# Performance work log

Hardware: AMD Instinct MI355X
Metric: run time of the kernel (lower is better)

The kernel has to match this reference:

```python
import jax, jax.numpy as jnp
import numpy as np

B, L = 8, 2048
H_IN = 20
K1, K2 = 16, 32
NG = 32            # n_gaussians
D1, D2 = 7, 5      # gaussian kernel input dims
DM = 128           # outer product out_features
DH = 32            # attribute embedding out_features
IDX_MAX = 8.0      # index_distance_max


def _gather(x, idx):
    # x: (B,L,H), idx: (B,L,K) -> (B,L,K,H)
    b = jnp.arange(x.shape[0])[:, None, None]
    return x[b, idx]


def _neighbors(frames, kmax):
    c = frames[:, :, 0, :]                      # centers (B,L,3)
    sq = jnp.sum(c * c, axis=-1)
    d2 = sq[:, :, None] + sq[:, None, :] - 2.0 * jnp.einsum('bld,bmd->blm', c, c)
    _, idx = jax.lax.top_k(-d2, kmax)           # self (d2=0) lands in slot 0
    return idx


def _coords(frames, seq_idx, idx):
    c = frames[:, :, 0, :]
    axes = frames[:, :, 1:4, :]                 # local frame axes of center node
    z = frames[:, :, 3, :]
    c_j = _gather(c, idx)
    z_j = _gather(z, idx)
    delta = c_j - c[:, :, None, :]              # (B,L,K,3)
    dist = jnp.sqrt(jnp.sum(delta * delta, -1, keepdims=True) + 1e-12)
    eucl = jnp.einsum('blkd,blad->blka', delta, axes)   # neighbor coords in local frame
    zdotz = jnp.sum(z[:, :, None, :] * z_j, -1, keepdims=True)
    deltadotz = jnp.sum(delta * z_j, -1, keepdims=True) / dist
    zdotdelta = jnp.sum(z[:, :, None, :] * delta, -1, keepdims=True) / dist
    sidx = seq_idx.astype(jnp.float32)          # (B,L,1)
    idist = jnp.clip(jnp.abs(_gather(sidx, idx) - sidx[:, :, None, :]), 0.0, IDX_MAX)
    return eucl, dist, zdotz, deltadotz, zdotdelta, idist


def _gaussian(x, centers, prec):
    # full-covariance Gaussian kernel: exp(-0.5 ||P_n (x - mu_n)||^2)
    diff = x[..., None] - centers               # (...,d,NG)
    y = jnp.einsum('...dn,dkn->...kn', diff, prec)
    return jnp.exp(-0.5 * jnp.sum(y * y, axis=-2))


def _forward(aa_attributes, aa_frame, aa_indices,
             gk1_centers, gk1_prec, op_kernel, op_bias,
             emb_W, emb_b, beta_W, beta_b, selfatt_W, selfatt_b,
             crossatt_W, crossatt_b, nodef_W, nodef_b,
             gk2_centers, gk2_prec, emb2_W, emb2_b):
    # --- neighborhood 1: euclidian + index_distance + ZdotZ + (DeltadotZ,ZdotDelta)
    idx1 = _neighbors(aa_frame, K1)
    eucl, _, zz, dz, zd, idist = _coords(aa_frame, aa_indices, idx1)
    coords1 = jnp.concatenate([eucl, idist, zz, dz, zd], axis=-1)   # (B,L,K1,7)
    neigh_attr = _gather(aa_attributes, idx1)                        # (B,L,K1,20)
    g1 = _gaussian(coords1, gk1_centers, gk1_prec)                   # (B,L,K1,NG)
    # outer-product embedding: sum over neighbors and (gaussian x attribute) pairs
    filt = jnp.einsum('blkg,blkh,gho->blo', g1, neigh_attr, op_kernel) + op_bias
    f = jax.nn.relu(filt)                                            # (B,L,128)
    emb = jax.nn.relu(f @ emb_W + emb_b)                             # (B,L,32)
    beta = jax.nn.relu(emb @ beta_W + beta_b)                        # (B,L,1)
    satt = jax.nn.relu(emb @ selfatt_W + selfatt_b)                  # (B,L,1)
    catt = jax.nn.relu(emb @ crossatt_W + crossatt_b)                # (B,L,1)
    nodef = jax.nn.relu(emb @ nodef_W + nodef_b)                     # (B,L,2)
    # --- neighborhood 2: distance + ZdotZ + (DeltadotZ,ZdotDelta) + index_distance
    idx2 = _neighbors(aa_frame, K2)
    _, dist2, zz2, dz2, zd2, idist2 = _coords(aa_frame, aa_indices, idx2)
    coords2 = jnp.concatenate([dist2, zz2, dz2, zd2, idist2], axis=-1)  # (B,L,K2,5)
    att_local = _gather(catt, idx2)                                  # (B,L,K2,1)
    nodef_local = _gather(nodef, idx2)                               # (B,L,K2,2)
    g2 = _gaussian(coords2, gk2_centers, gk2_prec)                   # (B,L,K2,NG)
    gw = jax.nn.relu(g2 @ emb2_W + emb2_b)                           # (B,L,K2,1)
    # --- graph attention aggregation (self slot is k=0)
    e = att_local.at[:, :, 0, :].set(satt)
    logits = beta[:, :, None, :] * e
    logits = logits - jnp.max(logits, axis=2, keepdims=True)
    w = gw * jnp.exp(logits)
    a = w / (jnp.sum(w, axis=2, keepdims=True) + 1e-6)               # (B,L,K2,1)
    out = jnp.sum(a * nodef_local, axis=2)                           # (B,L,2)
    return out


def setup_inputs():
    key = jax.random.key(0)
    ks = jax.random.split(key, 16)
    eye1 = jnp.tile(jnp.eye(D1, dtype=jnp.float32)[:, :, None], (1, 1, NG))
    eye2 = jnp.tile(jnp.eye(D2, dtype=jnp.float32)[:, :, None], (1, 1, NG))
    return {
        'aa_attributes': jax.random.normal(ks[0], (B, L, H_IN), jnp.float32),
        'aa_frame': jax.random.normal(ks[1], (B, L, 4, 3), jnp.float32),
        'aa_indices': jnp.arange(B * L, dtype=jnp.int32).reshape(B, L, 1),
        'gk1_centers': 0.1 * jax.random.normal(ks[2], (D1, NG), jnp.float32),
        'gk1_prec': eye1 + 0.05 * jax.random.normal(ks[3], (D1, D1, NG), jnp.float32),
        'op_kernel': 0.05 * jax.random.normal(ks[4], (NG, H_IN, DM), jnp.float32),
        'op_bias': jnp.zeros((DM,), jnp.float32),
        'emb_W': jax.random.normal(ks[5], (DM, DH), jnp.float32) / np.sqrt(DM),
        'emb_b': jnp.zeros((DH,), jnp.float32),
        'beta_W': jax.random.normal(ks[6], (DH, 1), jnp.float32) / np.sqrt(DH),
        'beta_b': jnp.zeros((1,), jnp.float32),
        'selfatt_W': jax.random.normal(ks[7], (DH, 1), jnp.float32) / np.sqrt(DH),
        'selfatt_b': jnp.zeros((1,), jnp.float32),
        'crossatt_W': jax.random.normal(ks[8], (DH, 1), jnp.float32) / np.sqrt(DH),
        'crossatt_b': jnp.zeros((1,), jnp.float32),
        'nodef_W': jax.random.normal(ks[9], (DH, 2), jnp.float32) / np.sqrt(DH),
        'nodef_b': jnp.zeros((2,), jnp.float32),
        'gk2_centers': 0.1 * jax.random.normal(ks[10], (D2, NG), jnp.float32),
        'gk2_prec': eye2 + 0.05 * jax.random.normal(ks[11], (D2, D2, NG), jnp.float32),
        'emb2_W': jax.random.normal(ks[12], (NG, 1), jnp.float32) / np.sqrt(NG),
        'emb2_b': jnp.zeros((1,), jnp.float32),
    }


def reference(aa_attributes, aa_frame, aa_indices,
              gk1_centers, gk1_prec, op_kernel, op_bias,
              emb_W, emb_b, beta_W, beta_b, selfatt_W, selfatt_b,
              crossatt_W, crossatt_b, nodef_W, nodef_b,
              gk2_centers, gk2_prec, emb2_W, emb2_b):
    return _forward(aa_attributes, aa_frame, aa_indices,
                    gk1_centers, gk1_prec, op_kernel, op_bias,
                    emb_W, emb_b, beta_W, beta_b, selfatt_W, selfatt_b,
                    crossatt_W, crossatt_b, nodef_W, nodef_b,
                    gk2_centers, gk2_prec, emb2_W, emb2_b)
```

## Files before the change

### kernel.cpp

```cpp
#include <hip/hip_runtime.h>

typedef unsigned int u32;
typedef unsigned long long u64;
typedef unsigned short u16;

#define NL 2048

typedef __attribute__((ext_vector_type(8))) short bf16x8;
typedef __attribute__((ext_vector_type(16))) float f32x16;

__device__ __forceinline__ u16 to_bf16(float f) {
  u32 b = __float_as_uint(f);
  b += 0x7FFFu + ((b >> 16) & 1u);
  return (u16)(b >> 16);
}

__device__ __forceinline__ void gload_lds16(const void* g, void* l) {
  __builtin_amdgcn_global_load_lds(
      (const __attribute__((address_space(1))) u32*)g,
      (__attribute__((address_space(3))) u32*)l, 16, 0, 0);
}

__device__ __forceinline__ u32 sort64_u32(u32 v, int lane) {
#pragma unroll
  for (int k = 2; k <= 64; k <<= 1) {
#pragma unroll
    for (int j = k >> 1; j > 0; j >>= 1) {
      u32 p = (u32)__shfl_xor((int)v, j, 64);
      bool lower = ((lane & j) == 0);
      bool asc = ((lane & k) == 0);
      u32 lo = v < p ? v : p;
      u32 hi = v < p ? p : v;
      v = (lower == asc) ? lo : hi;
    }
  }
  return v;
}

__global__ __launch_bounds__(512) void knn_prep_kernel(
    const float* __restrict__ frames, int* __restrict__ idx32,
    const float* __restrict__ opW, const float* __restrict__ embW,
    const float* __restrict__ betaW, const float* __restrict__ sattW,
    const float* __restrict__ cattW, const float* __restrict__ nodW,
    const float* __restrict__ betaB, const float* __restrict__ sattB,
    const float* __restrict__ cattB, const float* __restrict__ nodB,
    u16* __restrict__ opWt, u16* __restrict__ embWt, float* __restrict__ w5,
    float* __restrict__ b5) {
  __shared__ union U {
    struct {
      float4 cand[2048];
      u64 comp[8][256];
    } k;
    float tp[128 * 73];
  } sm;
  const int bx = blockIdx.x;
  const int tid = threadIdx.x;

  if (bx >= 2048) {
    if (bx < 2058) {
      const int k0 = (bx - 2048) * 64;
#pragma unroll
      for (int j = 0; j < 4; j++) {
        int f = tid + j * 512;
        int kk = f >> 5;
        int o4 = (f & 31) * 4;
        float4 v = *(const float4*)(opW + (size_t)(k0 + kk) * 128 + o4);
        sm.tp[(o4 + 0) * 73 + kk] = v.x;
        sm.tp[(o4 + 1) * 73 + kk] = v.y;
        sm.tp[(o4 + 2) * 73 + kk] = v.z;
        sm.tp[(o4 + 3) * 73 + kk] = v.w;
      }
      __syncthreads();
      u32* ow = (u32*)opWt;
#pragma unroll
      for (int j = 0; j < 8; j++) {
        int f = tid + j * 512;
        int o = f >> 5, q = f & 31;
        float lo = sm.tp[o * 73 + q * 2];
        float hi = sm.tp[o * 73 + q * 2 + 1];
        ow[o * 320 + (k0 >> 1) + q] = (u32)to_bf16(lo) | ((u32)to_bf16(hi) << 16);
      }
    } else {
      for (int f = tid; f < 4096; f += 512) {
        int j = f >> 7, kk = f & 127;
        embWt[f] = to_bf16(embW[(size_t)kk * 32 + j]);
      }
      if (tid < 160) {
        int h = tid >> 5, j = tid & 31;
        float v = (h == 0) ? betaW[j]
                  : (h == 1) ? sattW[j]
                  : (h == 2) ? cattW[j]
                  : (h == 3) ? nodW[j * 2]
                             : nodW[j * 2 + 1];
        w5[j * 8 + h] = v;
      } else if (tid < 165) {
        int h = tid - 160;
        float v = (h == 0) ? betaB[0]
                  : (h == 1) ? sattB[0]
                  : (h == 2) ? cattB[0]
                  : (h == 3) ? nodB[0]
                             : nodB[1];
        b5[h] = v;
      }
    }
    return;
  }

  const int w = tid >> 6, lane = tid & 63;
  const int query = bx * 8 + w;
  const int b = query >> 11, lq = query & (NL - 1);

#pragma unroll
  for (int i = 0; i < 4; i++) {
    int l = tid + i * 512;
    const float* fp = frames + (size_t)(b * NL + l) * 12;
    float4 fr = *(const float4*)fp;
    sm.k.cand[l] = make_float4(fr.x, fr.y, fr.z,
                               fr.x * fr.x + fr.y * fr.y + fr.z * fr.z);
  }
  __syncthreads();

  float4 me = sm.k.cand[lq];
  u32 k[32];
  u32 m = 0xFFFFFFFFu;
#pragma unroll
  for (int i = 0; i < 32; i++) {
    float4 c = sm.k.cand[i * 64 + lane];
    float dot = c.x * me.x + c.y * me.y + c.z * me.z;
    float d2 = (me.w + c.w) - 2.0f * dot;
    u32 kb = __float_as_uint(d2);
    u32 key = kb ^ ((u32)((int)kb >> 31) | 0x80000000u);
    k[i] = key;
    m = key < m ? key : m;
  }

  u32 ms = sort64_u32(m, lane);
  u32 T0 = (u32)__shfl((int)ms, 31, 64);

  int base = 0;
#pragma unroll
  for (int i = 0; i < 32; i++) {
    bool flag = (k[i] <= T0);
    u64 mask = __ballot(flag);
    if (flag) {
      u32 rank = __builtin_amdgcn_mbcnt_hi(
          (u32)(mask >> 32), __builtin_amdgcn_mbcnt_lo((u32)mask, 0u));
      int pos = base + (int)rank;
      if (pos < 256) sm.k.comp[w][pos] = ((u64)k[i] << 32) | (u32)(i * 64 + lane);
    }
    base += (int)__popcll(mask);
  }
  int cnt = base < 256 ? base : 256;
  __syncthreads();

  for (int b0 = 0; b0 < cnt; b0 += 64) {
    bool live = (b0 + lane < cnt);
    u64 e = live ? sm.k.comp[w][b0 + lane] : ~0ull;
    int r = 0;
    for (int mi = 0; mi < cnt; mi++) {
      u64 em = sm.k.comp[w][mi];
      r += (em < e) ? 1 : 0;
    }
    if (live && r < 32)
      idx32[(size_t)query * 32 + r] = (int)(e & 0xFFFFFFFFull);
  }
}

__global__ __launch_bounds__(256) void stage1_kernel(
    const float* __restrict__ frames, const float* __restrict__ attrs,
    const int* __restrict__ aaidx, const float* __restrict__ cen1,
    const float* __restrict__ prec1, const int* __restrict__ idx32,
    u16* __restrict__ outer) {
  __shared__ float sCoord[4 * 16 * 8];
  __shared__ float sAttrT[4 * 20 * 16];
  __shared__ float sG1T[4 * 32 * 17];
  const int tid = threadIdx.x;
  const int pt = tid >> 6, lane = tid & 63;
  const int pid = blockIdx.x * 4 + pt;
  const int b = pid >> 11;
  const int g = lane & 31;

  float pr[7][7], cn[7];
#pragma unroll
  for (int d = 0; d < 7; d++) {
    cn[d] = cen1[d * 32 + g];
#pragma unroll
    for (int kk = 0; kk < 7; kk++) pr[d][kk] = prec1[(d * 7 + kk) * 32 + g];
  }

  if (lane < 16) {
    int n = lane;
    int j = idx32[pid * 32 + n];
    int jg = b * NL + j;
    const float* fs = frames + (size_t)pid * 12;
    const float* fj = frames + (size_t)jg * 12;
    float4 A0 = *(const float4*)(fs);
    float4 A1 = *(const float4*)(fs + 4);
    float4 A2 = *(const float4*)(fs + 8);
    float4 B0 = *(const float4*)(fj);
    float4 B2 = *(const float4*)(fj + 8);
    float dx = B0.x - A0.x, dy = B0.y - A0.y, dzc = B0.z - A0.z;
    float a0x = A0.w, a0y = A1.x, a0z = A1.y;
    float a1x = A1.z, a1y = A1.w, a1z = A2.x;
    float a2x = A2.y, a2y = A2.z, a2z = A2.w;
    float zjx = B2.y, zjy = B2.z, zjz = B2.w;
    float dd = dx * dx + dy * dy + dzc * dzc + 1e-12f;
    float dist = sqrtf(dd);
    float e0 = dx * a0x + dy * a0y + dzc * a0z;
    float e1 = dx * a1x + dy * a1y + dzc * a1z;
    float e2 = dx * a2x + dy * a2y + dzc * a2z;
    float zz = a2x * zjx + a2y * zjy + a2z * zjz;
    float dzv = (dx * zjx + dy * zjy + dzc * zjz) / dist;
    float zdv = (a2x * dx + a2y * dy + a2z * dzc) / dist;
    float si = (float)aaidx[pid];
    float sj = (float)aaidx[jg];
    float idist = fminf(fabsf(sj - si), 8.0f);
    float* cr = sCoord + pt * 128 + n * 8;
    cr[0] = e0; cr[1] = e1; cr[2] = e2; cr[3] = idist;
    cr[4] = zz; cr[5] = dzv; cr[6] = zdv;
    const float* ar = attrs + (size_t)jg * 20;
    float4 q0 = *(const float4*)(ar);
    float4 q1 = *(const float4*)(ar + 4);
    float4 q2 = *(const float4*)(ar + 8);
    float4 q3 = *(const float4*)(ar + 12);
    float4 q4 = *(const float4*)(ar + 16);
    float av[20] = {q0.x, q0.y, q0.z, q0.w, q1.x, q1.y, q1.z, q1.w,
                    q2.x, q2.y, q2.z, q2.w, q3.x, q3.y, q3.z, q3.w,
                    q4.x, q4.y, q4.z, q4.w};
#pragma unroll
    for (int h = 0; h < 20; h++) sAttrT[pt * 320 + h * 16 + n] = av[h];
  }
  __syncthreads();
  {
    const int nh = lane >> 5;
#pragma unroll
    for (int i = 0; i < 8; i++) {
      int n = nh * 8 + i;
      const float* cr = sCoord + pt * 128 + n * 8;
      float df[7];
#pragma unroll
      for (int d = 0; d < 7; d++) df[d] = cr[d] - cn[d];
      float s = 0.0f;
#pragma unroll
      for (int kk = 0; kk < 7; kk++) {
        float y = 0.0f;
#pragma unroll
        for (int d = 0; d < 7; d++) y = fmaf(df[d], pr[d][kk], y);
        s = fmaf(y, y, s);
      }
      sG1T[pt * 544 + g * 17 + n] = __expf(-0.5f * s);
    }
  }
  __syncthreads();
  {
    const int hg = lane >> 5;
    float g16[16];
#pragma unroll
    for (int n = 0; n < 16; n++) g16[n] = sG1T[pt * 544 + g * 17 + n];
    u32* orow = (u32*)(outer + (size_t)pid * 640) + (g * 20 + hg * 10) / 2;
#pragma unroll
    for (int i = 0; i < 5; i++) {
      int h0 = hg * 10 + i * 2, h1 = h0 + 1;
      float a0 = 0.f, a1 = 0.f;
#pragma unroll
      for (int c = 0; c < 4; c++) {
        float4 v0 = *(float4*)&sAttrT[pt * 320 + h0 * 16 + c * 4];
        float4 v1 = *(float4*)&sAttrT[pt * 320 + h1 * 16 + c * 4];
        a0 = fmaf(v0.x, g16[c * 4 + 0], a0);
        a0 = fmaf(v0.y, g16[c * 4 + 1], a0);
        a0 = fmaf(v0.z, g16[c * 4 + 2], a0);
        a0 = fmaf(v0.w, g16[c * 4 + 3], a0);
        a1 = fmaf(v1.x, g16[c * 4 + 0], a1);
        a1 = fmaf(v1.y, g16[c * 4 + 1], a1);
        a1 = fmaf(v1.z, g16[c * 4 + 2], a1);
        a1 = fmaf(v1.w, g16[c * 4 + 3], a1);
      }
      orow[i] = (u32)to_bf16(a0) | ((u32)to_bf16(a1) << 16);
    }
  }
}

__global__ __launch_bounds__(256) void gemm_kernel(
    const u16* __restrict__ outer,
    const u16* __restrict__ opWt,
    const float* __restrict__ opB,
    const u16* __restrict__ embWt,
    const float* __restrict__ embB,
    const float* __restrict__ w5,
    const float* __restrict__ b5,
    float* __restrict__ head8) {
  __shared__ char smem[40960];
  const int tid = threadIdx.x;
  const int w = tid >> 6, lane = tid & 63;
  const int p0 = blockIdx.x * 32;
  const int lr = lane >> 3, lc = lane & 7;
  const int gsw = lc ^ lr;
  const int m = lane & 31, kh = lane >> 5;

  f32x16 acc;
#pragma unroll
  for (int r = 0; r < 16; r++) acc[r] = 0.f;

  const u16* gA = outer + (size_t)(p0 + w * 8 + lr) * 640 + gsw * 8;
#pragma unroll
  for (int cc = 0; cc < 10; cc++)
    gload_lds16(gA + cc * 64, smem + cc * 4096 + w * 1024);
  __syncthreads();

  const u16* gB = opWt + (size_t)(w * 32 + m) * 640;
#pragma unroll
  for (int cc = 0; cc < 10; cc++) {
#pragma unroll
    for (int s = 0; s < 4; s++) {
      int pg = (s * 2 + kh) ^ (m & 7);
      bf16x8 av = *(bf16x8*)(smem + cc * 4096 + m * 128 + pg * 16);
      bf16x8 bv = *(const bf16x8*)(gB + cc * 64 + s * 16 + kh * 8);
      acc = __builtin_amdgcn_mfma_f32_32x32x16_bf16(av, bv, acc, 0, 0, 0);
    }
  }
  __syncthreads();

  const int o = w * 32 + m;
  float bo = opB[o];
#pragma unroll
  for (int i = 0; i < 2; i++) {
    int j = w * 8 + i * 4 + (lane >> 4);
    int ge = (lane & 15) ^ (j & 7);
    gload_lds16(embWt + j * 128 + ge * 8, smem + 8192 + w * 2048 + i * 1024);
  }
  u16* sFb = (u16*)smem;
#pragma unroll
  for (int r = 0; r < 16; r++) {
    int mm = (r & 3) + 8 * (r >> 2) + 4 * kh;
    float v = fmaxf(acc[r] + bo, 0.f);
    int pg = (o >> 3) ^ (mm & 7);
    sFb[mm * 128 + pg * 8 + (o & 7)] = to_bf16(v);
  }
  __syncthreads();

  f32x16 acc2;
#pragma unroll
  for (int r = 0; r < 16; r++) acc2[r] = 0.f;
#pragma unroll
  for (int t2 = 0; t2 < 2; t2++) {
    int gg = (w * 2 + t2) * 2 + kh;
    int pg = gg ^ (m & 7);
    bf16x8 av = *(bf16x8*)(smem + m * 256 + pg * 16);
    bf16x8 bv = *(bf16x8*)(smem + 8192 + m * 256 + pg * 16);
    acc2 = __builtin_amdgcn_mfma_f32_32x32x16_bf16(av, bv, acc2, 0, 0, 0);
  }
  float* scr = (float*)(smem + 16384) + w * 1024;
#pragma unroll
  for (int r = 0; r < 16; r++) {
    int mm = (r & 3) + 8 * (r >> 2) + 4 * kh;
    scr[mm * 32 + m] = acc2[r];
  }
  __syncthreads();

  {
    float* sc = (float*)(smem + 16384);
    int i4 = tid * 4;
    float4 v0 = *(float4*)(sc + i4);
    float4 v1 = *(float4*)(sc + 1024 + i4);
    float4 v2 = *(float4*)(sc + 2048 + i4);
    float4 v3 = *(float4*)(sc + 3072 + i4);
    int pp = tid >> 3, j0 = (tid & 7) * 4;
    float4 eb = *(const float4*)(embB + j0);
    float4 e;
    e.x = fmaxf(v0.x + v1.x + v2.x + v3.x + eb.x, 0.f);
    e.y = fmaxf(v0.y + v1.y + v2.y + v3.y + eb.y, 0.f);
    e.z = fmaxf(v0.z + v1.z + v2.z + v3.z + eb.z, 0.f);
    e.w = fmaxf(v0.w + v1.w + v2.w + v3.w + eb.w, 0.f);
    *(float4*)((float*)smem + pp * 36 + j0) = e;
  }
  __syncthreads();

  if (tid < 160) {
    int h = tid >> 5, p = tid & 31;
    const float* sE = (const float*)smem + p * 36;
    float a = b5[h];
#pragma unroll
    for (int j = 0; j < 32; j++) a = fmaf(sE[j], w5[j * 8 + h], a);
    a = fmaxf(a, 0.f);
    int slot = (h < 2) ? (h + 4) : (h - 2);
    head8[(size_t)(p0 + p) * 8 + slot] = a;
  }
}

__global__ __launch_bounds__(256) void stage2_kernel(
    const float* __restrict__ frames, const int* __restrict__ aaidx,
    const float* __restrict__ cen2, const float* __restrict__ prec2,
    const float* __restrict__ emb2W, const float* __restrict__ emb2B,
    const int* __restrict__ idx32, const float* __restrict__ head8,
    float* __restrict__ out) {
  __shared__ float sCoord[4 * 32 * 5];
  __shared__ float sG2[4 * 32 * 33];
  const int tid = threadIdx.x;
  const int pt = tid >> 6, lane = tid & 63;
  const int pid = blockIdx.x * 4 + pt;
  const int b = pid >> 11;
  const int g = lane & 31;

  float pr[5][5], cn[5];
#pragma unroll
  for (int d = 0; d < 5; d++) {
    cn[d] = cen2[d * 32 + g];
#pragma unroll
    for (int kk = 0; kk < 5; kk++) pr[d][kk] = prec2[(d * 5 + kk) * 32 + g];
  }

  float4 hv = make_float4(0.f, 0.f, 0.f, 0.f);
  float betaS = 0.f, sattS = 0.f;
  if (lane < 32) {
    int n = lane;
    int j = idx32[pid * 32 + n];
    int jg = b * NL + j;
    const float* fs = frames + (size_t)pid * 12;
    const float* fj = frames + (size_t)jg * 12;
    float4 A0 = *(const float4*)(fs);
    float4 A2 = *(const float4*)(fs + 8);
    float4 B0 = *(const float4*)(fj);
    float4 B2 = *(const float4*)(fj + 8);
    float dx = B0.x - A0.x, dy = B0.y - A0.y, dzc = B0.z - A0.z;
    float a2x = A2.y, a2y = A2.z, a2z = A2.w;
    float zjx = B2.y, zjy = B2.z, zjz = B2.w;
    float dd = dx * dx + dy * dy + dzc * dzc + 1e-12f;
    float dist = sqrtf(dd);
    float zz = a2x * zjx + a2y * zjy + a2z * zjz;
    float dzv = (dx * zjx + dy * zjy + dzc * zjz) / dist;
    float zdv = (a2x * dx + a2y * dy + a2z * dzc) / dist;
    float si = (float)aaidx[pid];
    float sj = (float)aaidx[jg];
    float idist = fminf(fabsf(sj - si), 8.0f);
    float* cr = sCoord + pt * 160 + n * 5;
    cr[0] = dist; cr[1] = zz; cr[2] = dzv; cr[3] = zdv; cr[4] = idist;
    hv = *(const float4*)(head8 + (size_t)jg * 8);
    betaS = head8[(size_t)pid * 8 + 4];
    sattS = head8[(size_t)pid * 8 + 5];
  }
  __syncthreads();
  {
    const int nh = lane >> 5;
#pragma unroll
    for (int i = 0; i < 16; i++) {
      int n = nh * 16 + i;
      const float* cr = sCoord + pt * 160 + n * 5;
      float df[5];
#pragma unroll
      for (int d = 0; d < 5; d++) df[d] = cr[d] - cn[d];
      float s = 0.0f;
#pragma unroll
      for (int kk = 0; kk < 5; kk++) {
        float y = 0.0f;
#pragma unroll
        for (int d = 0; d < 5; d++) y = fmaf(df[d], pr[d][kk], y);
        s = fmaf(y, y, s);
      }
      sG2[pt * 1056 + n * 33 + g] = __expf(-0.5f * s);
    }
  }
  __syncthreads();
  if (lane < 32) {
    int n = lane;
    float gw = emb2B[0];
#pragma unroll 8
    for (int gg = 0; gg < 32; gg++)
      gw = fmaf(sG2[pt * 1056 + n * 33 + gg], emb2W[gg], gw);
    gw = fmaxf(gw, 0.0f);
    float e = (n == 0) ? sattS : hv.x;
    float logit = betaS * e;
    float mx = logit;
#pragma unroll
    for (int d = 1; d < 32; d <<= 1) mx = fmaxf(mx, __shfl_xor(mx, d, 64));
    float wv = gw * __expf(logit - mx);
    float S = wv;
#pragma unroll
    for (int d = 1; d < 32; d <<= 1) S += __shfl_xor(S, d, 64);
    float a = wv / (S + 1e-6f);
    float o0 = a * hv.y, o1 = a * hv.z;
#pragma unroll
    for (int d = 1; d < 32; d <<= 1) {
      o0 += __shfl_xor(o0, d, 64);
      o1 += __shfl_xor(o1, d, 64);
    }
    if (n == 0) {
      out[pid * 2 + 0] = o0;
      out[pid * 2 + 1] = o1;
    }
  }
}

extern "C" void kernel_launch(void* const* d_in, const int* in_sizes, int n_in,
                              void* d_out, int out_size, void* d_ws, size_t ws_size,
                              hipStream_t stream) {
  const float* attrs = (const float*)d_in[0];
  const float* frames = (const float*)d_in[1];
  const int* aaidx = (const int*)d_in[2];
  const float* cen1 = (const float*)d_in[3];
  const float* prec1 = (const float*)d_in[4];
  const float* opW = (const float*)d_in[5];
  const float* opB = (const float*)d_in[6];
  const float* embW = (const float*)d_in[7];
  const float* embB = (const float*)d_in[8];
  const float* betaW = (const float*)d_in[9];
  const float* betaB = (const float*)d_in[10];
  const float* sattW = (const float*)d_in[11];
  const float* sattB = (const float*)d_in[12];
  const float* cattW = (const float*)d_in[13];
  const float* cattB = (const float*)d_in[14];
  const float* nodW = (const float*)d_in[15];
  const float* nodB = (const float*)d_in[16];
  const float* cen2 = (const float*)d_in[17];
  const float* prec2 = (const float*)d_in[18];
  const float* emb2W = (const float*)d_in[19];
  const float* emb2B = (const float*)d_in[20];
  float* out = (float*)d_out;

  char* ws = (char*)d_ws;
  int* idx32 = (int*)ws;
  u16* outer_bf = (u16*)(ws + 2097152);
  float* head8 = (float*)(ws + 23068672);
  u16* opWt = (u16*)(ws + 23592960);
  u16* embWt = (u16*)(ws + 23756800);
  float* w5 = (float*)(ws + 23764992);
  float* b5 = (float*)(ws + 23766016);

  knn_prep_kernel<<<dim3(2059), dim3(512), 0, stream>>>(
      frames, idx32, opW, embW, betaW, sattW, cattW, nodW, betaB, sattB,
      cattB, nodB, opWt, embWt, w5, b5);
  stage1_kernel<<<dim3(4096), dim3(256), 0, stream>>>(frames, attrs, aaidx, cen1,
                                                      prec1, idx32, outer_bf);
  gemm_kernel<<<dim3(512), dim3(256), 0, stream>>>(outer_bf, opWt, opB, embWt,
                                                   embB, w5, b5, head8);
  stage2_kernel<<<dim3(4096), dim3(256), 0, stream>>>(frames, aaidx, cen2, prec2,
                                                      emb2W, emb2B, idx32, head8, out);
}
```

Measured before the change: 184.1 us.

## Fuse stage1 outer-product build into GEMM kernel and fast-path small kNN rank

Stage1 (gaussian kernel and outer product) now runs inside the GEMM kernel. Each block builds its 32 rows of the bf16 outer-product tile directly in swizzled LDS, which removes the roughly 21MB global write and re-read of the intermediate and one launch. The per-gaussian reduction over neighbors now uses per-lane partial sums combined with a cross-half shuffle. Separately, the kNN rank step gets a fully unrolled fast path for up to 64 candidates. The tradeoff is that the fused kernel launches only 512 blocks and runs 8 serialized iterations, each with two barriers, so the stage1 work has less parallelism.

```diff
diff --git a/kernel.cpp b/kernel.cpp
--- a/kernel.cpp
+++ b/kernel.cpp
@@ -153,174 +153,164 @@
   int cnt = base < 256 ? base : 256;
   __syncthreads();
 
-  for (int b0 = 0; b0 < cnt; b0 += 64) {
-    bool live = (b0 + lane < cnt);
-    u64 e = live ? sm.k.comp[w][b0 + lane] : ~0ull;
-    int r = 0;
-    for (int mi = 0; mi < cnt; mi++) {
+  if (cnt <= 64) {
+    int pz = cnt + lane;
+    if (pz < 64) sm.k.comp[w][pz] = ~0ull;
+    u64 e0 = sm.k.comp[w][lane];
+    int r0 = 0;
+#pragma unroll
+    for (int mi = 0; mi < 64; mi++) {
       u64 em = sm.k.comp[w][mi];
-      r += (em < e) ? 1 : 0;
-    }
-    if (live && r < 32)
-      idx32[(size_t)query * 32 + r] = (int)(e & 0xFFFFFFFFull);
-  }
-}
-
-__global__ __launch_bounds__(256) void stage1_kernel(
+      r0 += (em < e0) ? 1 : 0;
+    }
+    if (r0 < 32) idx32[(size_t)query * 32 + r0] = (int)(e0 & 0xFFFFFFFFull);
+  } else {
+    for (int b0 = 0; b0 < cnt; b0 += 64) {
+      bool live = (b0 + lane < cnt);
+      u64 e = live ? sm.k.comp[w][b0 + lane] : ~0ull;
+      int r = 0;
+      for (int mi = 0; mi < cnt; mi++) {
+        u64 em = sm.k.comp[w][mi];
+        r += (em < e) ? 1 : 0;
+      }
+      if (live && r < 32)
+        idx32[(size_t)query * 32 + r] = (int)(e & 0xFFFFFFFFull);
+    }
+  }
+}
+
+__global__ __launch_bounds__(256) void s1gemm_kernel(
     const float* __restrict__ frames, const float* __restrict__ attrs,
     const int* __restrict__ aaidx, const float* __restrict__ cen1,
     const float* __restrict__ prec1, const int* __restrict__ idx32,
-    u16* __restrict__ outer) {
-  __shared__ float sCoord[4 * 16 * 8];
-  __shared__ float sAttrT[4 * 20 * 16];
-  __shared__ float sG1T[4 * 32 * 17];
-  const int tid = threadIdx.x;
-  const int pt = tid >> 6, lane = tid & 63;
-  const int pid = blockIdx.x * 4 + pt;
-  const int b = pid >> 11;
-  const int g = lane & 31;
-
-  float pr[7][7], cn[7];
-#pragma unroll
-  for (int d = 0; d < 7; d++) {
-    cn[d] = cen1[d * 32 + g];
-#pragma unroll
-    for (int kk = 0; kk < 7; kk++) pr[d][kk] = prec1[(d * 7 + kk) * 32 + g];
-  }
-
-  if (lane < 16) {
-    int n = lane;
-    int j = idx32[pid * 32 + n];
-    int jg = b * NL + j;
-    const float* fs = frames + (size_t)pid * 12;
-    const float* fj = frames + (size_t)jg * 12;
-    float4 A0 = *(const float4*)(fs);
-    float4 A1 = *(const float4*)(fs + 4);
-    float4 A2 = *(const float4*)(fs + 8);
-    float4 B0 = *(const float4*)(fj);
-    float4 B2 = *(const float4*)(fj + 8);
-    float dx = B0.x - A0.x, dy = B0.y - A0.y, dzc = B0.z - A0.z;
-    float a0x = A0.w, a0y = A1.x, a0z = A1.y;
-    float a1x = A1.z, a1y = A1.w, a1z = A2.x;
-    float a2x = A2.y, a2y = A2.z, a2z = A2.w;
-    float zjx = B2.y, zjy = B2.z, zjz = B2.w;
-    float dd = dx * dx + dy * dy + dzc * dzc + 1e-12f;
-    float dist = sqrtf(dd);
-    float e0 = dx * a0x + dy * a0y + dzc * a0z;
-    float e1 = dx * a1x + dy * a1y + dzc * a1z;
-    float e2 = dx * a2x + dy * a2y + dzc * a2z;
-    float zz = a2x * zjx + a2y * zjy + a2z * zjz;
-    float dzv = (dx * zjx + dy * zjy + dzc * zjz) / dist;
-    float zdv = (a2x * dx + a2y * dy + a2z * dzc) / dist;
-    float si = (float)aaidx[pid];
-    float sj = (float)aaidx[jg];
-    float idist = fminf(fabsf(sj - si), 8.0f);
-    float* cr = sCoord + pt * 128 + n * 8;
-    cr[0] = e0; cr[1] = e1; cr[2] = e2; cr[3] = idist;
-    cr[4] = zz; cr[5] = dzv; cr[6] = zdv;
-    const float* ar = attrs + (size_t)jg * 20;
-    float4 q0 = *(const float4*)(ar);
-    float4 q1 = *(const float4*)(ar + 4);
-    float4 q2 = *(const float4*)(ar + 8);
-    float4 q3 = *(const float4*)(ar + 12);
-    float4 q4 = *(const float4*)(ar + 16);
-    float av[20] = {q0.x, q0.y, q0.z, q0.w, q1.x, q1.y, q1.z, q1.w,
-                    q2.x, q2.y, q2.z, q2.w, q3.x, q3.y, q3.z, q3.w,
-                    q4.x, q4.y, q4.z, q4.w};
-#pragma unroll
-    for (int h = 0; h < 20; h++) sAttrT[pt * 320 + h * 16 + n] = av[h];
-  }
-  __syncthreads();
-  {
-    const int nh = lane >> 5;
-#pragma unroll
-    for (int i = 0; i < 8; i++) {
-      int n = nh * 8 + i;
-      const float* cr = sCoord + pt * 128 + n * 8;
-      float df[7];
-#pragma unroll
-      for (int d = 0; d < 7; d++) df[d] = cr[d] - cn[d];
-      float s = 0.0f;
-#pragma unroll
-      for (int kk = 0; kk < 7; kk++) {
-        float y = 0.0f;
-#pragma unroll
-        for (int d = 0; d < 7; d++) y = fmaf(df[d], pr[d][kk], y);
-        s = fmaf(y, y, s);
-      }
-      sG1T[pt * 544 + g * 17 + n] = __expf(-0.5f * s);
-    }
-  }
-  __syncthreads();
-  {
-    const int hg = lane >> 5;
-    float g16[16];
-#pragma unroll
-    for (int n = 0; n < 16; n++) g16[n] = sG1T[pt * 544 + g * 17 + n];
-    u32* orow = (u32*)(outer + (size_t)pid * 640) + (g * 20 + hg * 10) / 2;
-#pragma unroll
-    for (int i = 0; i < 5; i++) {
-      int h0 = hg * 10 + i * 2, h1 = h0 + 1;
-      float a0 = 0.f, a1 = 0.f;
-#pragma unroll
-      for (int c = 0; c < 4; c++) {
-        float4 v0 = *(float4*)&sAttrT[pt * 320 + h0 * 16 + c * 4];
-        float4 v1 = *(float4*)&sAttrT[pt * 320 + h1 * 16 + c * 4];
-        a0 = fmaf(v0.x, g16[c * 4 + 0], a0);
-        a0 = fmaf(v0.y, g16[c * 4 + 1], a0);
-        a0 = fmaf(v0.z, g16[c * 4 + 2], a0);
-        a0 = fmaf(v0.w, g16[c * 4 + 3], a0);
-        a1 = fmaf(v1.x, g16[c * 4 + 0], a1);
-        a1 = fmaf(v1.y, g16[c * 4 + 1], a1);
-        a1 = fmaf(v1.z, g16[c * 4 + 2], a1);
-        a1 = fmaf(v1.w, g16[c * 4 + 3], a1);
-      }
-      orow[i] = (u32)to_bf16(a0) | ((u32)to_bf16(a1) << 16);
-    }
-  }
-}
-
-__global__ __launch_bounds__(256) void gemm_kernel(
-    const u16* __restrict__ outer,
-    const u16* __restrict__ opWt,
-    const float* __restrict__ opB,
-    const u16* __restrict__ embWt,
-    const float* __restrict__ embB,
-    const float* __restrict__ w5,
-    const float* __restrict__ b5,
+    const u16* __restrict__ opWt, const float* __restrict__ opB,
+    const u16* __restrict__ embWt, const float* __restrict__ embB,
+    const float* __restrict__ w5, const float* __restrict__ b5,
     float* __restrict__ head8) {
-  __shared__ char smem[40960];
+  __shared__ __align__(16) char smem[49152];
+  float* sCoord = (float*)(smem + 40960);
+  float* sAttrN = (float*)(smem + 43008);
   const int tid = threadIdx.x;
   const int w = tid >> 6, lane = tid & 63;
   const int p0 = blockIdx.x * 32;
-  const int lr = lane >> 3, lc = lane & 7;
-  const int gsw = lc ^ lr;
-  const int m = lane & 31, kh = lane >> 5;
-
+  const int g = lane & 31, nh = lane >> 5;
+
+  float pr[7][7], cn[7];
+#pragma unroll
+  for (int d = 0; d < 7; d++) {
+    cn[d] = cen1[d * 32 + g];
+#pragma unroll
+    for (int kk = 0; kk < 7; kk++) pr[d][kk] = prec1[(d * 7 + kk) * 32 + g];
+  }
+
+  for (int it = 0; it < 8; it++) {
+    __syncthreads();
+    const int m = w * 8 + it;
+    const int pid = p0 + m;
+    const int b = pid >> 11;
+    if (lane < 16) {
+      int n = lane;
+      int j = idx32[pid * 32 + n];
+      int jg = b * NL + j;
+      const float* fs = frames + (size_t)pid * 12;
+      const float* fj = frames + (size_t)jg * 12;
+      float4 A0 = *(const float4*)(fs);
+      float4 A1 = *(const float4*)(fs + 4);
+      float4 A2 = *(const float4*)(fs + 8);
+      float4 B0 = *(const float4*)(fj);
+      float4 B2 = *(const float4*)(fj + 8);
+      float dx = B0.x - A0.x, dy = B0.y - A0.y, dzc = B0.z - A0.z;
+      float a0x = A0.w, a0y = A1.x, a0z = A1.y;
+      float a1x = A1.z, a1y = A1.w, a1z = A2.x;
+      float a2x = A2.y, a2y = A2.z, a2z = A2.w;
+      float zjx = B2.y, zjy = B2.z, zjz = B2.w;
+      float dd = dx * dx + dy * dy + dzc * dzc + 1e-12f;
+      float dist = sqrtf(dd);
+      float e0 = dx * a0x + dy * a0y + dzc * a0z;
+      float e1 = dx * a1x + dy * a1y + dzc * a1z;
+      float e2 = dx * a2x + dy * a2y + dzc * a2z;
+      float zz = a2x * zjx + a2y * zjy + a2z * zjz;
+      float dzv = (dx * zjx + dy * zjy + dzc * zjz) / dist;
+      float zdv = (a2x * dx + a2y * dy + a2z * dzc) / dist;
+      float si = (float)aaidx[pid];
+      float sj = (float)aaidx[jg];
+      float idist = fminf(fabsf(sj - si), 8.0f);
+      float* cr = sCoord + w * 128 + n * 8;
+      cr[0] = e0; cr[1] = e1; cr[2] = e2; cr[3] = idist;
+      cr[4] = zz; cr[5] = dzv; cr[6] = zdv;
+      const float* ar = attrs + (size_t)jg * 20;
+      float* aw = sAttrN + w * 320 + n * 20;
+      *(float4*)(aw + 0) = *(const float4*)(ar + 0);
+      *(float4*)(aw + 4) = *(const float4*)(ar + 4);
+      *(float4*)(aw + 8) = *(const float4*)(ar + 8);
+      *(float4*)(aw + 12) = *(const float4*)(ar + 12);
+      *(float4*)(aw + 16) = *(const float4*)(ar + 16);
+    }
+    __syncthreads();
+    float partial[20];
+#pragma unroll
+    for (int h = 0; h < 20; h++) partial[h] = 0.f;
+#pragma unroll
+    for (int q = 0; q < 8; q++) {
+      int n = nh * 8 + q;
+      const float* cr = sCoord + w * 128 + n * 8;
+      float4 c0 = *(const float4*)(cr);
+      float4 c1 = *(const float4*)(cr + 4);
+      float df[7] = {c0.x - cn[0], c0.y - cn[1], c0.z - cn[2], c0.w - cn[3],
+                     c1.x - cn[4], c1.y - cn[5], c1.z - cn[6]};
+      float s = 0.0f;
+#pragma unroll
+      for (int kk = 0; kk < 7; kk++) {
+        float y = 0.0f;
+#pragma unroll
+        for (int d = 0; d < 7; d++) y = fmaf(df[d], pr[d][kk], y);
+        s = fmaf(y, y, s);
+      }
+      float gval = __expf(-0.5f * s);
+      const float* ar = sAttrN + w * 320 + n * 20;
+      float4 a0 = *(const float4*)(ar + 0);
+      float4 a1 = *(const float4*)(ar + 4);
+      float4 a2 = *(const float4*)(ar + 8);
+      float4 a3 = *(const float4*)(ar + 12);
+      float4 a4 = *(const float4*)(ar + 16);
+      float av[20] = {a0.x, a0.y, a0.z, a0.w, a1.x, a1.y, a1.z, a1.w,
+                      a2.x, a2.y, a2.z, a2.w, a3.x, a3.y, a3.z, a3.w,
+                      a4.x, a4.y, a4.z, a4.w};
+#pragma unroll
+      for (int h = 0; h < 20; h++) partial[h] = fmaf(gval, av[h], partial[h]);
+    }
+#pragma unroll
+    for (int h = 0; h < 20; h++)
+      partial[h] += __shfl_xor(partial[h], 32, 64);
+#pragma unroll
+    for (int i = 0; i < 5; i++) {
+      int h = nh * 10 + i * 2;
+      int o = g * 20 + h;
+      int cc = o >> 6, G = (o >> 3) & 7, e = o & 7;
+      u32 pk = (u32)to_bf16(partial[h]) | ((u32)to_bf16(partial[h + 1]) << 16);
+      *(u32*)(smem + cc * 4096 + m * 128 + ((G ^ (m & 7)) << 4) + e * 2) = pk;
+    }
+  }
+  __syncthreads();
+
+  const int m2 = lane & 31, kh = lane >> 5;
   f32x16 acc;
 #pragma unroll
   for (int r = 0; r < 16; r++) acc[r] = 0.f;
-
-  const u16* gA = outer + (size_t)(p0 + w * 8 + lr) * 640 + gsw * 8;
-#pragma unroll
-  for (int cc = 0; cc < 10; cc++)
-    gload_lds16(gA + cc * 64, smem + cc * 4096 + w * 1024);
-  __syncthreads();
-
-  const u16* gB = opWt + (size_t)(w * 32 + m) * 640;
+  const u16* gB = opWt + (size_t)(w * 32 + m2) * 640;
 #pragma unroll
   for (int cc = 0; cc < 10; cc++) {
 #pragma unroll
     for (int s = 0; s < 4; s++) {
-      int pg = (s * 2 + kh) ^ (m & 7);
-      bf16x8 av = *(bf16x8*)(smem + cc * 4096 + m * 128 + pg * 16);
+      int pg = (s * 2 + kh) ^ (m2 & 7);
+      bf16x8 av = *(bf16x8*)(smem + cc * 4096 + m2 * 128 + pg * 16);
       bf16x8 bv = *(const bf16x8*)(gB + cc * 64 + s * 16 + kh * 8);
       acc = __builtin_amdgcn_mfma_f32_32x32x16_bf16(av, bv, acc, 0, 0, 0);
     }
   }
   __syncthreads();
 
-  const int o = w * 32 + m;
+  const int o = w * 32 + m2;
   float bo = opB[o];
 #pragma unroll
   for (int i = 0; i < 2; i++) {
@@ -344,16 +334,16 @@
 #pragma unroll
   for (int t2 = 0; t2 < 2; t2++) {
     int gg = (w * 2 + t2) * 2 + kh;
-    int pg = gg ^ (m & 7);
-    bf16x8 av = *(bf16x8*)(smem + m * 256 + pg * 16);
-    bf16x8 bv = *(bf16x8*)(smem + 8192 + m * 256 + pg * 16);
+    int pg = gg ^ (m2 & 7);
+    bf16x8 av = *(bf16x8*)(smem + m2 * 256 + pg * 16);
+    bf16x8 bv = *(bf16x8*)(smem + 8192 + m2 * 256 + pg * 16);
     acc2 = __builtin_amdgcn_mfma_f32_32x32x16_bf16(av, bv, acc2, 0, 0, 0);
   }
   float* scr = (float*)(smem + 16384) + w * 1024;
 #pragma unroll
   for (int r = 0; r < 16; r++) {
     int mm = (r & 3) + 8 * (r >> 2) + 4 * kh;
-    scr[mm * 32 + m] = acc2[r];
+    scr[mm * 32 + m2] = acc2[r];
   }
   __syncthreads();
 
@@ -518,20 +508,18 @@
 
   char* ws = (char*)d_ws;
   int* idx32 = (int*)ws;
-  u16* outer_bf = (u16*)(ws + 2097152);
-  float* head8 = (float*)(ws + 23068672);
-  u16* opWt = (u16*)(ws + 23592960);
-  u16* embWt = (u16*)(ws + 23756800);
-  float* w5 = (float*)(ws + 23764992);
-  float* b5 = (float*)(ws + 23766016);
+  float* head8 = (float*)(ws + 2097152);
+  u16* opWt = (u16*)(ws + 2621440);
+  u16* embWt = (u16*)(ws + 2785280);
+  float* w5 = (float*)(ws + 2793472);
+  float* b5 = (float*)(ws + 2794496);
 
   knn_prep_kernel<<<dim3(2059), dim3(512), 0, stream>>>(
       frames, idx32, opW, embW, betaW, sattW, cattW, nodW, betaB, sattB,
       cattB, nodB, opWt, embWt, w5, b5);
-  stage1_kernel<<<dim3(4096), dim3(256), 0, stream>>>(frames, attrs, aaidx, cen1,
-                                                      prec1, idx32, outer_bf);
-  gemm_kernel<<<dim3(512), dim3(256), 0, stream>>>(outer_bf, opWt, opB, embWt,
-                                                   embB, w5, b5, head8);
+  s1gemm_kernel<<<dim3(512), dim3(256), 0, stream>>>(
+      frames, attrs, aaidx, cen1, prec1, idx32, opWt, opB, embWt, embB, w5,
+      b5, head8);
   stage2_kernel<<<dim3(4096), dim3(256), 0, stream>>>(frames, aaidx, cen2, prec2,
                                                       emb2W, emb2B, idx32, head8, out);
 }
```

After: 191.2 us. 1.04x slower.
